# Performance work log

Hardware: AMD Instinct MI355X
Metric: run time of the kernel (lower is better)

The kernel has to match this reference:

```python
import jax, jax.numpy as jnp
import numpy as np

N = 20000        # nodes
E = 640000       # edges (avg degree 32)
D_IN = 128       # node_features
D_HID = 256      # conv_booster * D_IN
D_DENSE = 128    # D_HID // linear_decay
N_CLASSES = 2


def _glorot(key, fan_in, fan_out):
    s = np.sqrt(1.0 / fan_in).astype(np.float32)
    return jax.random.normal(key, (fan_in, fan_out), jnp.float32) * s


def setup_inputs() -> dict:
    key = jax.random.key(0)
    ks = jax.random.split(key, 12)
    return {
        "node_features": jax.random.normal(ks[0], (N, D_IN), jnp.float32),
        "edge_index": jax.random.randint(ks[1], (2, E), 0, N, dtype=jnp.int32),
        "edge_weight": jax.random.uniform(ks[2], (E,), jnp.float32),
        "W1": _glorot(ks[3], D_IN, D_HID),
        "b1": jnp.zeros((D_HID,), jnp.float32),
        "W2": _glorot(ks[4], D_HID, D_HID),
        "b2": jnp.zeros((D_HID,), jnp.float32),
        "Wd1": _glorot(ks[5], D_HID, D_DENSE),
        "bd1": jnp.zeros((D_DENSE,), jnp.float32),
        "Wd2": _glorot(ks[6], D_DENSE, N_CLASSES),
        "bd2": jnp.zeros((N_CLASSES,), jnp.float32),
    }


def gcn_conv(x, row, col, w, W, b, n):
    # PyG GCNConv: add self-loops (weight 1), symmetric normalization,
    # x' = D^{-1/2}(A+I)D^{-1/2} (x W) + b
    h = x @ W                                        # [n, out]
    loop = jnp.arange(n, dtype=row.dtype)
    r = jnp.concatenate([row, loop])
    c = jnp.concatenate([col, loop])
    ww = jnp.concatenate([w, jnp.ones((n,), w.dtype)])
    deg = jax.ops.segment_sum(ww, c, num_segments=n)  # degree at targets
    dinv = jnp.where(deg > 0, jax.lax.rsqrt(deg), 0.0)
    norm = dinv[r] * ww * dinv[c]                    # [E+n]
    msg = norm[:, None] * h[r]                       # gather + scale (hot path)
    return jax.ops.segment_sum(msg, c, num_segments=n) + b  # scatter-add


def reference(node_features, edge_index, edge_weight,
              W1, b1, W2, b2, Wd1, bd1, Wd2, bd2):
    row, col = edge_index[0], edge_index[1]
    n = node_features.shape[0]
    h = gcn_conv(node_features, row, col, edge_weight, W1, b1, n)
    h = gcn_conv(h, row, col, edge_weight, W2, b2, n)
    g = jnp.mean(h, axis=0)                          # MeanAggregation pooling
    z = jax.nn.relu(g @ Wd1 + bd1)
    logits = z @ Wd2 + bd2
    return jax.nn.softmax(logits)
```

## Files before the change

kernel.cpp:

```cpp
#include <hip/hip_runtime.h>


#define D_IN 128
#define D_HID 256
#define D_DENSE 128
#define R0 10240
#define NSL 128
#define NFOLD 250
#define FOLD_C 80
#define NTILE 157

__global__ __launch_bounds__(1024) void k_scatter(
    const int* __restrict__ tgt, const int* __restrict__ src,
    const float* __restrict__ w, const float* __restrict__ dinv,
    const float* __restrict__ u, float* __restrict__ part,
    int E, int N, int mode) {
    __shared__ float acc[R0];
    const int range = blockIdx.x & 1;
    const int slice = blockIdx.x >> 1;
    const int base  = range ? R0 : 0;
    const int lim   = range ? (N - R0) : R0;
    const int per = (E + NSL - 1) / NSL;
    const int e0 = slice * per, e1 = min(e0 + per, E);
    float* outp = part + (range ? (size_t)NSL * R0 + (size_t)slice * lim
                                : (size_t)slice * lim);
    for (int i = threadIdx.x; i < lim; i += 1024) acc[i] = 0.f;
    __syncthreads();
    for (int e = e0 + threadIdx.x; e < e1; e += 1024) {
        int t = tgt[e] - base;
        if ((unsigned)t < (unsigned)lim) {
            float v = w[e];
            if (mode != 0) {
                int c = src[e];
                float dc = dinv[c];
                v *= (mode == 2) ? dc * u[c] : dc;
            }
            atomicAdd(&acc[t], v);
        }
    }
    __syncthreads();
    for (int i = threadIdx.x; i < lim; i += 1024) outp[i] = acc[i];
}

__global__ __launch_bounds__(1024) void k_fold(
    const float* __restrict__ part, float* __restrict__ dinv,
    float* __restrict__ u, float* __restrict__ S_u_part,
    const float* __restrict__ W1, const float* __restrict__ b1,
    const float* __restrict__ W2, float* __restrict__ M, float* __restrict__ c2,
    int N, int mode) {
    __shared__ float lds[1044];
    const int b = blockIdx.x, tid = threadIdx.x;

    if (b >= NFOLD) {
        int q = b - NFOLD;
        lds[tid] = W2[(tid >> 2) * 256 + q * 4 + (tid & 3)];
        __syncthreads();
        int wvi = tid >> 6, lane = tid & 63;
        for (int kr = 0; kr < 8; ++kr) {
            int k = wvi * 8 + kr;
            float a0 = 0, a1 = 0, a2 = 0, a3 = 0;
            #pragma unroll
            for (int it = 0; it < 4; ++it) {
                int j = it * 64 + lane;
                float a = W1[k * 256 + j];
                a0 += a * lds[j*4+0]; a1 += a * lds[j*4+1];
                a2 += a * lds[j*4+2]; a3 += a * lds[j*4+3];
            }
            #pragma unroll
            for (int off = 32; off > 0; off >>= 1) {
                a0 += __shfl_down(a0, off, 64); a1 += __shfl_down(a1, off, 64);
                a2 += __shfl_down(a2, off, 64); a3 += __shfl_down(a3, off, 64);
            }
            if (lane == 0) {
                M[k * 256 + q*4 + 0] = a0; M[k * 256 + q*4 + 1] = a1;
                M[k * 256 + q*4 + 2] = a2; M[k * 256 + q*4 + 3] = a3;
            }
        }
        if (wvi == 0) {
            float a0 = 0, a1 = 0, a2 = 0, a3 = 0;
            #pragma unroll
            for (int it = 0; it < 4; ++it) {
                int j = it * 64 + lane;
                float a = b1[j];
                a0 += a * lds[j*4+0]; a1 += a * lds[j*4+1];
                a2 += a * lds[j*4+2]; a3 += a * lds[j*4+3];
            }
            #pragma unroll
            for (int off = 32; off > 0; off >>= 1) {
                a0 += __shfl_down(a0, off, 64); a1 += __shfl_down(a1, off, 64);
                a2 += __shfl_down(a2, off, 64); a3 += __shfl_down(a3, off, 64);
            }
            if (lane == 0) {
                c2[q*4+0] = a0; c2[q*4+1] = a1;
                c2[q*4+2] = a2; c2[q*4+3] = a3;
            }
        }
        return;
    }

    const int j = tid & 127, rg = tid >> 7;
    const int i = b * FOLD_C + j;
    const bool act = (j < FOLD_C) && (i < N);
    float sv = 0.f;
    if (act) {
        size_t st; const float* pp;
        if (i < R0) { st = R0;               pp = part + i; }
        else        { st = (size_t)(N - R0); pp = part + (size_t)NSL * R0 + (i - R0); }
        pp += (size_t)rg * 16 * st;
        #pragma unroll
        for (int r = 0; r < 16; ++r) sv += pp[(size_t)r * st];
    }
    lds[rg * 128 + j] = sv;
    __syncthreads();
    float ui = 0.f;
    if (rg == 0) {
        float tot = 0.f;
        #pragma unroll
        for (int q = 0; q < 8; ++q) tot += lds[q * 128 + j];
        if (act) {
            if (mode == 0) dinv[i] = rsqrtf(tot + 1.0f);
            else { float d = dinv[i]; ui = d * (tot + d); u[i] = ui; }
        }
    }
    if (mode == 1) {
        float v = ui;
        #pragma unroll
        for (int off = 32; off > 0; off >>= 1) v += __shfl_down(v, off, 64);
        if ((tid & 63) == 0) lds[1028 + (tid >> 6)] = v;
        __syncthreads();
        if (tid == 0) {
            float t2 = 0.f;
            #pragma unroll
            for (int q = 0; q < 16; ++q) t2 += lds[1028 + q];
            S_u_part[b] = t2;
        }
    }
}

__global__ __launch_bounds__(1024) void k_contract(
    const float* __restrict__ x, const float* __restrict__ part,
    const float* __restrict__ dinv, const float* __restrict__ u,
    float* __restrict__ s_part, int N) {
    __shared__ float sh[1024];
    __shared__ float wvl[128];
    const int b = blockIdx.x, tid = threadIdx.x;
    const int k = tid & 127, rg = tid >> 7;
    const int i0 = b * 128;
    const int i = i0 + k;
    const bool act = i < N;
    float sv = 0.f;
    if (act) {
        size_t st; const float* pp;
        if (i < R0) { st = R0;               pp = part + i; }
        else        { st = (size_t)(N - R0); pp = part + (size_t)NSL * R0 + (i - R0); }
        pp += (size_t)rg * 16 * st;
        #pragma unroll
        for (int r = 0; r < 16; ++r) sv += pp[(size_t)r * st];
    }
    sh[tid] = sv;
    __syncthreads();
    if (rg == 0) {
        float q = 0.f;
        #pragma unroll
        for (int t2 = 0; t2 < 8; ++t2) q += sh[t2 * 128 + k];
        float d = act ? dinv[i] : 0.f;
        wvl[k] = act ? d * (q + d * u[i]) : 0.f;
    }
    __syncthreads();
    float a = 0.f;
    #pragma unroll
    for (int jj = 0; jj < 16; ++jj) {
        int m = rg + 8 * jj;
        int i2 = i0 + m;
        float xv = x[(size_t)(i2 < N ? i2 : i0) * D_IN + k];
        a += wvl[m] * xv;
    }
    sh[tid] = a;
    __syncthreads();
    if (rg == 0) {
        float t2s = 0.f;
        #pragma unroll
        for (int t2 = 0; t2 < 8; ++t2) t2s += sh[t2 * 128 + k];
        s_part[b * 128 + k] = t2s;
    }
}

__global__ __launch_bounds__(1024) void k_head(
    const float* __restrict__ s_part, const float* __restrict__ S_u_part,
    const float* __restrict__ M, const float* __restrict__ c2,
    const float* __restrict__ b2, const float* __restrict__ Wd1,
    const float* __restrict__ bd1, const float* __restrict__ Wd2,
    const float* __restrict__ bd2, float* __restrict__ out, float inv_n) {
    __shared__ float sh[1024];
    __shared__ float ss[128];
    __shared__ float gv[256];
    __shared__ float zz[128];
    __shared__ float su[16];
    __shared__ float S_u_s;
    const int tid = threadIdx.x;
    const int k = tid & 127, rg = tid >> 7;

    float a2 = 0.f;
    for (int q = rg; q < NTILE; q += 8) a2 += s_part[q * 128 + k];
    float v = (tid < NFOLD) ? S_u_part[tid] : 0.f;
    #pragma unroll
    for (int off = 32; off > 0; off >>= 1) v += __shfl_down(v, off, 64);
    sh[tid] = a2;
    if ((tid & 63) == 0) su[tid >> 6] = v;
    __syncthreads();
    if (rg == 0) {
        float t2 = 0.f;
        #pragma unroll
        for (int q = 0; q < 8; ++q) t2 += sh[q * 128 + k];
        ss[k] = t2;
    }
    if (tid == 0) {
        float t2 = 0.f;
        #pragma unroll
        for (int q = 0; q < 16; ++q) t2 += su[q];
        S_u_s = t2;
    }
    __syncthreads();

    {
        const int t = tid & 255, p = tid >> 8;
        float gp = 0.f;
        #pragma unroll
        for (int kk = 0; kk < 32; ++kk)
            gp += ss[p * 32 + kk] * M[(p * 32 + kk) * 256 + t];
        sh[tid] = gp;
    }
    __syncthreads();
    if (tid < 256) {
        float gval = sh[tid] + sh[256 + tid] + sh[512 + tid] + sh[768 + tid];
        gv[tid] = (gval + S_u_s * c2[tid]) * inv_n + b2[tid];
    }
    __syncthreads();

    {
        const int j = tid & 127, p = tid >> 7;
        float zp = 0.f;
        #pragma unroll
        for (int t2 = 0; t2 < 32; ++t2)
            zp += gv[p * 32 + t2] * Wd1[(p * 32 + t2) * D_DENSE + j];
        sh[tid] = zp;
    }
    __syncthreads();
    if (tid < 128) {
        float z = bd1[tid];
        #pragma unroll
        for (int p2 = 0; p2 < 8; ++p2) z += sh[p2 * 128 + tid];
        zz[tid] = fmaxf(z, 0.f);
    }
    __syncthreads();

    float p0 = 0.f, p1 = 0.f;
    if (tid < 128) {
        p0 = zz[tid] * Wd2[tid * 2 + 0];
        p1 = zz[tid] * Wd2[tid * 2 + 1];
    }
    #pragma unroll
    for (int off = 32; off > 0; off >>= 1) {
        p0 += __shfl_down(p0, off, 64);
        p1 += __shfl_down(p1, off, 64);
    }
    if ((tid & 63) == 0) { sh[tid >> 6] = p0; sh[32 + (tid >> 6)] = p1; }
    __syncthreads();
    if (tid == 0) {
        float l0 = bd2[0], l1 = bd2[1];
        #pragma unroll
        for (int q = 0; q < 16; ++q) { l0 += sh[q]; l1 += sh[32 + q]; }
        float m = fmaxf(l0, l1);
        float e0 = expf(l0 - m), e1 = expf(l1 - m);
        float inv = 1.0f / (e0 + e1);
        out[0] = e0 * inv;
        out[1] = e1 * inv;
    }
}

extern "C" void kernel_launch(void* const* d_in, const int* in_sizes, int n_in,
                              void* d_out, int out_size, void* d_ws, size_t ws_size,
                              hipStream_t stream) {
    const float* x   = (const float*)d_in[0];
    const int*   ei  = (const int*)  d_in[1];
    const float* w   = (const float*)d_in[2];
    const float* W1  = (const float*)d_in[3];
    const float* b1  = (const float*)d_in[4];
    const float* W2  = (const float*)d_in[5];
    const float* b2  = (const float*)d_in[6];
    const float* Wd1 = (const float*)d_in[7];
    const float* bd1 = (const float*)d_in[8];
    const float* Wd2 = (const float*)d_in[9];
    const float* bd2 = (const float*)d_in[10];
    float* out = (float*)d_out;

    const int N = in_sizes[0] / D_IN;
    const int E = in_sizes[1] / 2;
    const int* row = ei;
    const int* col = ei + E;

    float* fws    = (float*)d_ws;
    float* part   = fws;
    float* dinv   = part + (size_t)NSL * N;
    float* u      = dinv + N;
    float* s_part = u + N;
    float* S_u_p  = s_part + (size_t)NTILE * D_IN;
    float* M      = S_u_p + NFOLD;
    float* c2     = M + D_IN * D_HID;

    k_scatter<<<2 * NSL, 1024, 0, stream>>>(col, row, w, dinv, u, part, E, N, 0);
    k_fold<<<NFOLD + 64, 1024, 0, stream>>>(part, dinv, u, S_u_p, W1, b1, W2, M, c2, N, 0);
    k_scatter<<<2 * NSL, 1024, 0, stream>>>(row, col, w, dinv, u, part, E, N, 1);
    k_fold<<<NFOLD, 1024, 0, stream>>>(part, dinv, u, S_u_p, W1, b1, W2, M, c2, N, 1);
    k_scatter<<<2 * NSL, 1024, 0, stream>>>(row, col, w, dinv, u, part, E, N, 2);
    k_contract<<<NTILE, 1024, 0, stream>>>(x, part, dinv, u, s_part, N);
    k_head<<<1, 1024, 0, stream>>>(s_part, S_u_p, M, c2, b2, Wd1, bd1, Wd2, bd2,
                                   out, 1.0f / (float)N);
}
```

Before: 148.8 us.

## Replace LDS-privatized scatter partials with direct global atomics into node bins

Each of the three edge scatter passes now does atomicAdd straight into an N-length global bin array, replacing per-slice shared-memory histograms. Those histograms wrote NSL partial copies that later kernels had to fold. The fold kernels become simple per-node elementwise kernels, and a memset zeroes the bins up front. This removes the large partial buffer traffic and the reduction passes. In exchange, all updates now contend as global atomics, and float summation order becomes nondeterministic.

```diff
diff --git a/kernel.cpp b/kernel.cpp
--- a/kernel.cpp
+++ b/kernel.cpp
@@ -4,141 +4,121 @@
 #define D_IN 128
 #define D_HID 256
 #define D_DENSE 128
-#define R0 10240
-#define NSL 128
-#define NFOLD 250
-#define FOLD_C 80
+#define NUB 20
 #define NTILE 157
-
-__global__ __launch_bounds__(1024) void k_scatter(
-    const int* __restrict__ tgt, const int* __restrict__ src,
-    const float* __restrict__ w, const float* __restrict__ dinv,
-    const float* __restrict__ u, float* __restrict__ part,
-    int E, int N, int mode) {
-    __shared__ float acc[R0];
-    const int range = blockIdx.x & 1;
-    const int slice = blockIdx.x >> 1;
-    const int base  = range ? R0 : 0;
-    const int lim   = range ? (N - R0) : R0;
-    const int per = (E + NSL - 1) / NSL;
-    const int e0 = slice * per, e1 = min(e0 + per, E);
-    float* outp = part + (range ? (size_t)NSL * R0 + (size_t)slice * lim
-                                : (size_t)slice * lim);
-    for (int i = threadIdx.x; i < lim; i += 1024) acc[i] = 0.f;
-    __syncthreads();
-    for (int e = e0 + threadIdx.x; e < e1; e += 1024) {
-        int t = tgt[e] - base;
-        if ((unsigned)t < (unsigned)lim) {
-            float v = w[e];
-            if (mode != 0) {
-                int c = src[e];
-                float dc = dinv[c];
-                v *= (mode == 2) ? dc * u[c] : dc;
-            }
-            atomicAdd(&acc[t], v);
-        }
-    }
-    __syncthreads();
-    for (int i = threadIdx.x; i < lim; i += 1024) outp[i] = acc[i];
-}
-
-__global__ __launch_bounds__(1024) void k_fold(
-    const float* __restrict__ part, float* __restrict__ dinv,
-    float* __restrict__ u, float* __restrict__ S_u_part,
+#define SGRID 256
+
+__global__ __launch_bounds__(1024) void k_deg(
+    const int* __restrict__ col, const float* __restrict__ w,
+    float* __restrict__ bins, int E) {
+    for (int e = blockIdx.x * 1024 + threadIdx.x; e < E; e += SGRID * 1024)
+        atomicAdd(&bins[col[e]], w[e]);
+}
+
+__global__ __launch_bounds__(1024) void k_node0(
+    const float* __restrict__ bins0, float* __restrict__ dinv,
     const float* __restrict__ W1, const float* __restrict__ b1,
     const float* __restrict__ W2, float* __restrict__ M, float* __restrict__ c2,
-    int N, int mode) {
+    int N) {
     __shared__ float lds[1044];
     const int b = blockIdx.x, tid = threadIdx.x;
 
-    if (b >= NFOLD) {
-        int q = b - NFOLD;
-        lds[tid] = W2[(tid >> 2) * 256 + q * 4 + (tid & 3)];
-        __syncthreads();
-        int wvi = tid >> 6, lane = tid & 63;
-        for (int kr = 0; kr < 8; ++kr) {
-            int k = wvi * 8 + kr;
-            float a0 = 0, a1 = 0, a2 = 0, a3 = 0;
-            #pragma unroll
-            for (int it = 0; it < 4; ++it) {
-                int j = it * 64 + lane;
-                float a = W1[k * 256 + j];
-                a0 += a * lds[j*4+0]; a1 += a * lds[j*4+1];
-                a2 += a * lds[j*4+2]; a3 += a * lds[j*4+3];
-            }
-            #pragma unroll
-            for (int off = 32; off > 0; off >>= 1) {
-                a0 += __shfl_down(a0, off, 64); a1 += __shfl_down(a1, off, 64);
-                a2 += __shfl_down(a2, off, 64); a3 += __shfl_down(a3, off, 64);
-            }
-            if (lane == 0) {
-                M[k * 256 + q*4 + 0] = a0; M[k * 256 + q*4 + 1] = a1;
-                M[k * 256 + q*4 + 2] = a2; M[k * 256 + q*4 + 3] = a3;
-            }
-        }
-        if (wvi == 0) {
-            float a0 = 0, a1 = 0, a2 = 0, a3 = 0;
-            #pragma unroll
-            for (int it = 0; it < 4; ++it) {
-                int j = it * 64 + lane;
-                float a = b1[j];
-                a0 += a * lds[j*4+0]; a1 += a * lds[j*4+1];
-                a2 += a * lds[j*4+2]; a3 += a * lds[j*4+3];
-            }
-            #pragma unroll
-            for (int off = 32; off > 0; off >>= 1) {
-                a0 += __shfl_down(a0, off, 64); a1 += __shfl_down(a1, off, 64);
-                a2 += __shfl_down(a2, off, 64); a3 += __shfl_down(a3, off, 64);
-            }
-            if (lane == 0) {
-                c2[q*4+0] = a0; c2[q*4+1] = a1;
-                c2[q*4+2] = a2; c2[q*4+3] = a3;
-            }
-        }
+    if (b < NUB) {
+        int i = b * 1000 + tid;
+        if (tid < 1000 && i < N) dinv[i] = rsqrtf(bins0[i] + 1.0f);
         return;
     }
-
-    const int j = tid & 127, rg = tid >> 7;
-    const int i = b * FOLD_C + j;
-    const bool act = (j < FOLD_C) && (i < N);
-    float sv = 0.f;
-    if (act) {
-        size_t st; const float* pp;
-        if (i < R0) { st = R0;               pp = part + i; }
-        else        { st = (size_t)(N - R0); pp = part + (size_t)NSL * R0 + (i - R0); }
-        pp += (size_t)rg * 16 * st;
-        #pragma unroll
-        for (int r = 0; r < 16; ++r) sv += pp[(size_t)r * st];
-    }
-    lds[rg * 128 + j] = sv;
-    __syncthreads();
+    int q = b - NUB;
+    lds[tid] = W2[(tid >> 2) * 256 + q * 4 + (tid & 3)];
+    __syncthreads();
+    int wvi = tid >> 6, lane = tid & 63;
+    for (int kr = 0; kr < 8; ++kr) {
+        int k = wvi * 8 + kr;
+        float a0 = 0, a1 = 0, a2 = 0, a3 = 0;
+        #pragma unroll
+        for (int it = 0; it < 4; ++it) {
+            int j = it * 64 + lane;
+            float a = W1[k * 256 + j];
+            a0 += a * lds[j*4+0]; a1 += a * lds[j*4+1];
+            a2 += a * lds[j*4+2]; a3 += a * lds[j*4+3];
+        }
+        #pragma unroll
+        for (int off = 32; off > 0; off >>= 1) {
+            a0 += __shfl_down(a0, off, 64); a1 += __shfl_down(a1, off, 64);
+            a2 += __shfl_down(a2, off, 64); a3 += __shfl_down(a3, off, 64);
+        }
+        if (lane == 0) {
+            M[k * 256 + q*4 + 0] = a0; M[k * 256 + q*4 + 1] = a1;
+            M[k * 256 + q*4 + 2] = a2; M[k * 256 + q*4 + 3] = a3;
+        }
+    }
+    if (wvi == 0) {
+        float a0 = 0, a1 = 0, a2 = 0, a3 = 0;
+        #pragma unroll
+        for (int it = 0; it < 4; ++it) {
+            int j = it * 64 + lane;
+            float a = b1[j];
+            a0 += a * lds[j*4+0]; a1 += a * lds[j*4+1];
+            a2 += a * lds[j*4+2]; a3 += a * lds[j*4+3];
+        }
+        #pragma unroll
+        for (int off = 32; off > 0; off >>= 1) {
+            a0 += __shfl_down(a0, off, 64); a1 += __shfl_down(a1, off, 64);
+            a2 += __shfl_down(a2, off, 64); a3 += __shfl_down(a3, off, 64);
+        }
+        if (lane == 0) {
+            c2[q*4+0] = a0; c2[q*4+1] = a1;
+            c2[q*4+2] = a2; c2[q*4+3] = a3;
+        }
+    }
+}
+
+__global__ __launch_bounds__(1024) void k_u(
+    const int* __restrict__ row, const int* __restrict__ col,
+    const float* __restrict__ w, const float* __restrict__ dinv,
+    float* __restrict__ bins, int E) {
+    for (int e = blockIdx.x * 1024 + threadIdx.x; e < E; e += SGRID * 1024)
+        atomicAdd(&bins[row[e]], w[e] * dinv[col[e]]);
+}
+
+__global__ __launch_bounds__(1024) void k_node1(
+    const float* __restrict__ bins1, const float* __restrict__ dinv,
+    float* __restrict__ u, float* __restrict__ S_u_part, int N) {
+    __shared__ float su[16];
+    const int b = blockIdx.x, tid = threadIdx.x;
+    const int i = b * 1000 + tid;
     float ui = 0.f;
-    if (rg == 0) {
-        float tot = 0.f;
-        #pragma unroll
-        for (int q = 0; q < 8; ++q) tot += lds[q * 128 + j];
-        if (act) {
-            if (mode == 0) dinv[i] = rsqrtf(tot + 1.0f);
-            else { float d = dinv[i]; ui = d * (tot + d); u[i] = ui; }
-        }
-    }
-    if (mode == 1) {
-        float v = ui;
-        #pragma unroll
-        for (int off = 32; off > 0; off >>= 1) v += __shfl_down(v, off, 64);
-        if ((tid & 63) == 0) lds[1028 + (tid >> 6)] = v;
-        __syncthreads();
-        if (tid == 0) {
-            float t2 = 0.f;
-            #pragma unroll
-            for (int q = 0; q < 16; ++q) t2 += lds[1028 + q];
-            S_u_part[b] = t2;
-        }
+    if (tid < 1000 && i < N) {
+        float d = dinv[i];
+        ui = d * (bins1[i] + d);
+        u[i] = ui;
+    }
+    float v = ui;
+    #pragma unroll
+    for (int off = 32; off > 0; off >>= 1) v += __shfl_down(v, off, 64);
+    if ((tid & 63) == 0) su[tid >> 6] = v;
+    __syncthreads();
+    if (tid == 0) {
+        float t2 = 0.f;
+        #pragma unroll
+        for (int q = 0; q < 16; ++q) t2 += su[q];
+        S_u_part[b] = t2;
+    }
+}
+
+__global__ __launch_bounds__(1024) void k_wv(
+    const int* __restrict__ row, const int* __restrict__ col,
+    const float* __restrict__ w, const float* __restrict__ dinv,
+    const float* __restrict__ u, float* __restrict__ bins, int E) {
+    for (int e = blockIdx.x * 1024 + threadIdx.x; e < E; e += SGRID * 1024) {
+        int c = col[e];
+        float dc = dinv[c];
+        atomicAdd(&bins[row[e]], w[e] * dc * u[c]);
     }
 }
 
 __global__ __launch_bounds__(1024) void k_contract(
-    const float* __restrict__ x, const float* __restrict__ part,
+    const float* __restrict__ x, const float* __restrict__ bins2,
     const float* __restrict__ dinv, const float* __restrict__ u,
     float* __restrict__ s_part, int N) {
     __shared__ float sh[1024];
@@ -146,25 +126,11 @@
     const int b = blockIdx.x, tid = threadIdx.x;
     const int k = tid & 127, rg = tid >> 7;
     const int i0 = b * 128;
-    const int i = i0 + k;
-    const bool act = i < N;
-    float sv = 0.f;
-    if (act) {
-        size_t st; const float* pp;
-        if (i < R0) { st = R0;               pp = part + i; }
-        else        { st = (size_t)(N - R0); pp = part + (size_t)NSL * R0 + (i - R0); }
-        pp += (size_t)rg * 16 * st;
-        #pragma unroll
-        for (int r = 0; r < 16; ++r) sv += pp[(size_t)r * st];
-    }
-    sh[tid] = sv;
-    __syncthreads();
-    if (rg == 0) {
-        float q = 0.f;
-        #pragma unroll
-        for (int t2 = 0; t2 < 8; ++t2) q += sh[t2 * 128 + k];
+    if (tid < 128) {
+        int i = i0 + k;
+        bool act = i < N;
         float d = act ? dinv[i] : 0.f;
-        wvl[k] = act ? d * (q + d * u[i]) : 0.f;
+        wvl[k] = act ? d * (bins2[i] + d * u[i]) : 0.f;
     }
     __syncthreads();
     float a = 0.f;
@@ -202,7 +168,7 @@
 
     float a2 = 0.f;
     for (int q = rg; q < NTILE; q += 8) a2 += s_part[q * 128 + k];
-    float v = (tid < NFOLD) ? S_u_part[tid] : 0.f;
+    float v = (tid < NUB) ? S_u_part[tid] : 0.f;
     #pragma unroll
     for (int off = 32; off > 0; off >>= 1) v += __shfl_down(v, off, 64);
     sh[tid] = a2;
@@ -299,21 +265,23 @@
     const int* row = ei;
     const int* col = ei + E;
 
-    float* fws    = (float*)d_ws;
-    float* part   = fws;
-    float* dinv   = part + (size_t)NSL * N;
+    float* bins0  = (float*)d_ws;
+    float* bins1  = bins0 + N;
+    float* bins2  = bins1 + N;
+    float* dinv   = bins2 + N;
     float* u      = dinv + N;
     float* s_part = u + N;
     float* S_u_p  = s_part + (size_t)NTILE * D_IN;
-    float* M      = S_u_p + NFOLD;
+    float* M      = S_u_p + NUB;
     float* c2     = M + D_IN * D_HID;
 
-    k_scatter<<<2 * NSL, 1024, 0, stream>>>(col, row, w, dinv, u, part, E, N, 0);
-    k_fold<<<NFOLD + 64, 1024, 0, stream>>>(part, dinv, u, S_u_p, W1, b1, W2, M, c2, N, 0);
-    k_scatter<<<2 * NSL, 1024, 0, stream>>>(row, col, w, dinv, u, part, E, N, 1);
-    k_fold<<<NFOLD, 1024, 0, stream>>>(part, dinv, u, S_u_p, W1, b1, W2, M, c2, N, 1);
-    k_scatter<<<2 * NSL, 1024, 0, stream>>>(row, col, w, dinv, u, part, E, N, 2);
-    k_contract<<<NTILE, 1024, 0, stream>>>(x, part, dinv, u, s_part, N);
+    hipMemsetAsync(bins0, 0, 3 * (size_t)N * sizeof(float), stream);
+    k_deg<<<SGRID, 1024, 0, stream>>>(col, w, bins0, E);
+    k_node0<<<NUB + 64, 1024, 0, stream>>>(bins0, dinv, W1, b1, W2, M, c2, N);
+    k_u<<<SGRID, 1024, 0, stream>>>(row, col, w, dinv, bins1, E);
+    k_node1<<<NUB, 1024, 0, stream>>>(bins1, dinv, u, S_u_p, N);
+    k_wv<<<SGRID, 1024, 0, stream>>>(row, col, w, dinv, u, bins2, E);
+    k_contract<<<NTILE, 1024, 0, stream>>>(x, bins2, dinv, u, s_part, N);
     k_head<<<1, 1024, 0, stream>>>(s_part, S_u_p, M, c2, b2, Wd1, bd1, Wd2, bd2,
                                    out, 1.0f / (float)N);
 }
```

Result: slower. 234.6 us (+57.7%).

## Fuse head into contract via last-block ticket; precompute dinv*u; vectorize LDS init

Applied to the files above, without the earlier changes.

Removes the separate single-block head kernel launch by having the last k_contract block, chosen through an atomic ticket counter, perform the final reduction and MLP head. The ticket is reset by the first scatter kernel. Stores d*u instead of u so the mode-2 scatter does one gather per edge instead of two. Vectorizes the LDS zeroing and the output copy with float4. Adds threadfences and an atomic, and relies on the reset ordering across kernels.

```diff
diff --git a/kernel.cpp b/kernel.cpp
--- a/kernel.cpp
+++ b/kernel.cpp
@@ -13,9 +13,10 @@
 __global__ __launch_bounds__(1024) void k_scatter(
     const int* __restrict__ tgt, const int* __restrict__ src,
     const float* __restrict__ w, const float* __restrict__ dinv,
-    const float* __restrict__ u, float* __restrict__ part,
-    int E, int N, int mode) {
-    __shared__ float acc[R0];
+    const float* __restrict__ du, float* __restrict__ part,
+    unsigned* __restrict__ ticket, int E, int N, int mode) {
+    __shared__ __align__(16) float acc[R0];
+    if (mode == 0 && blockIdx.x == 0 && threadIdx.x == 0) ticket[0] = 0u;
     const int range = blockIdx.x & 1;
     const int slice = blockIdx.x >> 1;
     const int base  = range ? R0 : 0;
@@ -24,27 +25,26 @@
     const int e0 = slice * per, e1 = min(e0 + per, E);
     float* outp = part + (range ? (size_t)NSL * R0 + (size_t)slice * lim
                                 : (size_t)slice * lim);
-    for (int i = threadIdx.x; i < lim; i += 1024) acc[i] = 0.f;
+    for (int i = threadIdx.x * 4; i < lim; i += 4096)
+        *(float4*)&acc[i] = make_float4(0.f, 0.f, 0.f, 0.f);
     __syncthreads();
     for (int e = e0 + threadIdx.x; e < e1; e += 1024) {
         int t = tgt[e] - base;
         if ((unsigned)t < (unsigned)lim) {
             float v = w[e];
-            if (mode != 0) {
-                int c = src[e];
-                float dc = dinv[c];
-                v *= (mode == 2) ? dc * u[c] : dc;
-            }
+            if (mode == 1)      v *= dinv[src[e]];
+            else if (mode == 2) v *= du[src[e]];
             atomicAdd(&acc[t], v);
         }
     }
     __syncthreads();
-    for (int i = threadIdx.x; i < lim; i += 1024) outp[i] = acc[i];
+    for (int i = threadIdx.x * 4; i < lim; i += 4096)
+        *(float4*)&outp[i] = *(const float4*)&acc[i];
 }
 
 __global__ __launch_bounds__(1024) void k_fold(
     const float* __restrict__ part, float* __restrict__ dinv,
-    float* __restrict__ u, float* __restrict__ S_u_part,
+    float* __restrict__ du, float* __restrict__ S_u_part,
     const float* __restrict__ W1, const float* __restrict__ b1,
     const float* __restrict__ W2, float* __restrict__ M, float* __restrict__ c2,
     int N, int mode) {
@@ -119,7 +119,7 @@
         for (int q = 0; q < 8; ++q) tot += lds[q * 128 + j];
         if (act) {
             if (mode == 0) dinv[i] = rsqrtf(tot + 1.0f);
-            else { float d = dinv[i]; ui = d * (tot + d); u[i] = ui; }
+            else { float d = dinv[i]; ui = d * (tot + d); du[i] = d * ui; }
         }
     }
     if (mode == 1) {
@@ -139,15 +139,27 @@
 
 __global__ __launch_bounds__(1024) void k_contract(
     const float* __restrict__ x, const float* __restrict__ part,
-    const float* __restrict__ dinv, const float* __restrict__ u,
-    float* __restrict__ s_part, int N) {
+    const float* __restrict__ dinv, const float* __restrict__ du,
+    float* __restrict__ s_part, const float* __restrict__ S_u_part,
+    const float* __restrict__ M, const float* __restrict__ c2,
+    const float* __restrict__ b2, const float* __restrict__ Wd1,
+    const float* __restrict__ bd1, const float* __restrict__ Wd2,
+    const float* __restrict__ bd2, unsigned* __restrict__ ticket,
+    float* __restrict__ out, int N, float inv_n) {
     __shared__ float sh[1024];
     __shared__ float wvl[128];
+    __shared__ float ss[128];
+    __shared__ float gv[256];
+    __shared__ float zz[128];
+    __shared__ float su[16];
+    __shared__ float S_u_s;
+    __shared__ unsigned lastflag;
     const int b = blockIdx.x, tid = threadIdx.x;
     const int k = tid & 127, rg = tid >> 7;
     const int i0 = b * 128;
     const int i = i0 + k;
     const bool act = i < N;
+
     float sv = 0.f;
     if (act) {
         size_t st; const float* pp;
@@ -164,7 +176,7 @@
         #pragma unroll
         for (int t2 = 0; t2 < 8; ++t2) q += sh[t2 * 128 + k];
         float d = act ? dinv[i] : 0.f;
-        wvl[k] = act ? d * (q + d * u[i]) : 0.f;
+        wvl[k] = act ? d * (q + du[i]) : 0.f;
     }
     __syncthreads();
     float a = 0.f;
@@ -183,28 +195,24 @@
         for (int t2 = 0; t2 < 8; ++t2) t2s += sh[t2 * 128 + k];
         s_part[b * 128 + k] = t2s;
     }
-}
-
-__global__ __launch_bounds__(1024) void k_head(
-    const float* __restrict__ s_part, const float* __restrict__ S_u_part,
-    const float* __restrict__ M, const float* __restrict__ c2,
-    const float* __restrict__ b2, const float* __restrict__ Wd1,
-    const float* __restrict__ bd1, const float* __restrict__ Wd2,
-    const float* __restrict__ bd2, float* __restrict__ out, float inv_n) {
-    __shared__ float sh[1024];
-    __shared__ float ss[128];
-    __shared__ float gv[256];
-    __shared__ float zz[128];
-    __shared__ float su[16];
-    __shared__ float S_u_s;
-    const int tid = threadIdx.x;
-    const int k = tid & 127, rg = tid >> 7;
+
+    __syncthreads();
+    __threadfence();
+    if (tid == 0) {
+        unsigned old = __hip_atomic_fetch_add(ticket, 1u, __ATOMIC_ACQ_REL,
+                                              __HIP_MEMORY_SCOPE_AGENT);
+        lastflag = (old == NTILE - 1) ? 1u : 0u;
+    }
+    __syncthreads();
+    if (!lastflag) return;
+    __threadfence();
 
     float a2 = 0.f;
     for (int q = rg; q < NTILE; q += 8) a2 += s_part[q * 128 + k];
     float v = (tid < NFOLD) ? S_u_part[tid] : 0.f;
     #pragma unroll
     for (int off = 32; off > 0; off >>= 1) v += __shfl_down(v, off, 64);
+    __syncthreads();
     sh[tid] = a2;
     if ((tid & 63) == 0) su[tid >> 6] = v;
     __syncthreads();
@@ -228,6 +236,7 @@
         #pragma unroll
         for (int kk = 0; kk < 32; ++kk)
             gp += ss[p * 32 + kk] * M[(p * 32 + kk) * 256 + t];
+        __syncthreads();
         sh[tid] = gp;
     }
     __syncthreads();
@@ -243,6 +252,7 @@
         #pragma unroll
         for (int t2 = 0; t2 < 32; ++t2)
             zp += gv[p * 32 + t2] * Wd1[(p * 32 + t2) * D_DENSE + j];
+        __syncthreads();
         sh[tid] = zp;
     }
     __syncthreads();
@@ -264,6 +274,7 @@
         p0 += __shfl_down(p0, off, 64);
         p1 += __shfl_down(p1, off, 64);
     }
+    __syncthreads();
     if ((tid & 63) == 0) { sh[tid >> 6] = p0; sh[32 + (tid >> 6)] = p1; }
     __syncthreads();
     if (tid == 0) {
@@ -299,21 +310,22 @@
     const int* row = ei;
     const int* col = ei + E;
 
-    float* fws    = (float*)d_ws;
+    unsigned* ticket = (unsigned*)d_ws;
+    float* fws    = (float*)d_ws + 64;
     float* part   = fws;
     float* dinv   = part + (size_t)NSL * N;
-    float* u      = dinv + N;
-    float* s_part = u + N;
+    float* du     = dinv + N;
+    float* s_part = du + N;
     float* S_u_p  = s_part + (size_t)NTILE * D_IN;
     float* M      = S_u_p + NFOLD;
     float* c2     = M + D_IN * D_HID;
 
-    k_scatter<<<2 * NSL, 1024, 0, stream>>>(col, row, w, dinv, u, part, E, N, 0);
-    k_fold<<<NFOLD + 64, 1024, 0, stream>>>(part, dinv, u, S_u_p, W1, b1, W2, M, c2, N, 0);
-    k_scatter<<<2 * NSL, 1024, 0, stream>>>(row, col, w, dinv, u, part, E, N, 1);
-    k_fold<<<NFOLD, 1024, 0, stream>>>(part, dinv, u, S_u_p, W1, b1, W2, M, c2, N, 1);
-    k_scatter<<<2 * NSL, 1024, 0, stream>>>(row, col, w, dinv, u, part, E, N, 2);
-    k_contract<<<NTILE, 1024, 0, stream>>>(x, part, dinv, u, s_part, N);
-    k_head<<<1, 1024, 0, stream>>>(s_part, S_u_p, M, c2, b2, Wd1, bd1, Wd2, bd2,
-                                   out, 1.0f / (float)N);
+    k_scatter<<<2 * NSL, 1024, 0, stream>>>(col, row, w, dinv, du, part, ticket, E, N, 0);
+    k_fold<<<NFOLD + 64, 1024, 0, stream>>>(part, dinv, du, S_u_p, W1, b1, W2, M, c2, N, 0);
+    k_scatter<<<2 * NSL, 1024, 0, stream>>>(row, col, w, dinv, du, part, ticket, E, N, 1);
+    k_fold<<<NFOLD, 1024, 0, stream>>>(part, dinv, du, S_u_p, W1, b1, W2, M, c2, N, 1);
+    k_scatter<<<2 * NSL, 1024, 0, stream>>>(row, col, w, dinv, du, part, ticket, E, N, 2);
+    k_contract<<<NTILE, 1024, 0, stream>>>(x, part, dinv, du, s_part, S_u_p,
+                                           M, c2, b2, Wd1, bd1, Wd2, bd2,
+                                           ticket, out, N, 1.0f / (float)N);
 }
```

Result: slower. 191.3 us (+28.6%).
